# Optimization experiments

Measured on AMD Instinct MI355X. Metric: run time of the kernel, lower is better.

The kernel has to match this reference:

```python
import jax, jax.numpy as jnp
import numpy as np

EMBED_DIM = 1024
NUM_HEADS = 16
HEAD_DIM = EMBED_DIM // NUM_HEADS
SCALING = HEAD_DIM ** -0.5


def setup_inputs() -> dict:
    key = jax.random.key(0)
    ks = jax.random.split(key, 10)
    B, S, D = 2, 2048, EMBED_DIM
    lim = 1.0 / np.sqrt(D)  # torch Linear default init scale
    def lin(k):
        kw, kb = jax.random.split(k)
        W = jax.random.uniform(kw, (D, D), jnp.float32, -lim, lim)
        b = jax.random.uniform(kb, (D,), jnp.float32, -lim, lim)
        return W, b
    Wq, bq = lin(ks[0])
    Wk, bk = lin(ks[1])
    Wv, bv = lin(ks[2])
    Wo, bo = lin(ks[3])
    hidden_states = jax.random.normal(ks[4], (B, S, D), jnp.float32)
    attention_mask = jnp.ones((B, S), jnp.int32)  # unused by the module's forward
    return {"hidden_states": hidden_states, "attention_mask": attention_mask,
            "Wq": Wq, "bq": bq, "Wk": Wk, "bk": bk, "Wv": Wv, "bv": bv,
            "Wo": Wo, "bo": bo}


def reference(hidden_states, attention_mask, Wq, bq, Wk, bk, Wv, bv, Wo, bo):
    B, S, D = hidden_states.shape
    H, hd = NUM_HEADS, HEAD_DIM

    def split_heads(x):  # [B,S,D] -> [B,H,S,hd]
        return x.reshape(B, S, H, hd).transpose(0, 2, 1, 3)

    q = split_heads(hidden_states @ Wq.T + bq) * SCALING
    k = split_heads(hidden_states @ Wk.T + bk)
    v = split_heads(hidden_states @ Wv.T + bv)

    scores = jnp.einsum("bhqd,bhkd->bhqk", q, k)  # [B,H,S,S]
    mask_value = jnp.finfo(scores.dtype).min
    causal = jnp.triu(jnp.ones((S, S), bool), k=1)  # True above diagonal
    scores = jnp.where(causal, mask_value, scores)
    probs = jax.nn.softmax(scores, axis=-1)

    out = jnp.einsum("bhqk,bhkd->bhqd", probs, v)  # [B,H,S,hd]
    out = out.transpose(0, 2, 1, 3).reshape(B, S, D)
    return out @ Wo.T + bo
```

## Files before the change

kernel.cpp:

```cpp
#include <hip/hip_runtime.h>


typedef __bf16 bf16;
typedef __attribute__((ext_vector_type(8))) __bf16 bf16x8;
typedef __attribute__((ext_vector_type(4))) __bf16 bf16x4;
typedef __attribute__((ext_vector_type(4))) float f32x4;

#define MFMA16(a, b, c) __builtin_amdgcn_mfma_f32_16x16x32_bf16((a), (b), (c), 0, 0, 0)

__device__ __forceinline__ void gl_lds16(const bf16* g, bf16* l) {
  __builtin_amdgcn_global_load_lds(
      (__attribute__((address_space(1))) void*)g,
      (__attribute__((address_space(3))) void*)l, 16, 0, 0);
}

__global__ __launch_bounds__(256) void cvt5(
    const float* __restrict__ x, const float* __restrict__ wq,
    const float* __restrict__ wk, const float* __restrict__ wv,
    const float* __restrict__ wo,
    bf16* __restrict__ xb, bf16* __restrict__ wqb, bf16* __restrict__ wkb,
    bf16* __restrict__ wvb, bf16* __restrict__ wob) {
  const int bx = blockIdx.x;
  const float* s;
  bf16* d;
  int base;
  if (bx < 4096)      { s = x;  d = xb;  base = bx; }
  else if (bx < 5120) { s = wq; d = wqb; base = bx - 4096; }
  else if (bx < 6144) { s = wk; d = wkb; base = bx - 5120; }
  else if (bx < 7168) { s = wv; d = wvb; base = bx - 6144; }
  else                { s = wo; d = wob; base = bx - 7168; }
  const int i = base * 1024 + threadIdx.x * 4;
  const float4 v = *(const float4*)(s + i);
  bf16x4 o;
  o[0] = (bf16)v.x; o[1] = (bf16)v.y; o[2] = (bf16)v.z; o[3] = (bf16)v.w;
  *(bf16x4*)(d + i) = o;
}

__global__ __launch_bounds__(256) void vtrans(const bf16* __restrict__ v,
                                              bf16* __restrict__ vt) {
  __shared__ bf16 Ts[64 * 80];
  const int t = threadIdx.x;
  const int st = blockIdx.x;
  const int bh = blockIdx.y;
  const int bb = bh >> 4, h = bh & 15;
  const bf16* src = v + ((size_t)bb * 2048 + st * 64) * 1024 + h * 64;
#pragma unroll
  for (int i = 0; i < 2; ++i) {
    const int idx = i * 256 + t;
    const int sl = idx >> 3, c = idx & 7;
    *(bf16x8*)&Ts[sl * 80 + c * 8] = *(const bf16x8*)(src + (size_t)sl * 1024 + c * 8);
  }
  __syncthreads();
  bf16* dst = vt + (size_t)bh * 64 * 2048 + st * 64;
#pragma unroll
  for (int i = 0; i < 2; ++i) {
    const int idx = i * 256 + t;
    const int d = idx >> 3, c2 = idx & 7;
    bf16x8 tmp;
#pragma unroll
    for (int e = 0; e < 8; ++e) tmp[e] = Ts[(c2 * 8 + e) * 80 + d];
    *(bf16x8*)(dst + (size_t)d * 2048 + c2 * 8) = tmp;
  }
}

template <int BM, typename OutT>
__global__ __launch_bounds__(256, 2) void gemm_bt3(
    const bf16* __restrict__ A,
    const bf16* __restrict__ W0, const bf16* __restrict__ W1, const bf16* __restrict__ W2,
    const float* __restrict__ B0, const float* __restrict__ B1, const float* __restrict__ B2,
    OutT* __restrict__ O0, OutT* __restrict__ O1, OutT* __restrict__ O2,
    float s0, float s1, float s2, int K) {
  constexpr int WM = BM / 32;
  __shared__ bf16 As[BM * 64];
  __shared__ bf16 Bs[128 * 64];

  const int t = threadIdx.x;
  const int lane = t & 63;
  const int wv = t >> 6;
  const int wm = wv & 1, wn = wv >> 1;
  const int qd = lane >> 4, ln = lane & 15;

  const int which = blockIdx.x >> 3;
  const bf16* W = (which == 0) ? W0 : (which == 1) ? W1 : W2;
  const float* Bi = (which == 0) ? B0 : (which == 1) ? B1 : B2;
  OutT* O = (which == 0) ? O0 : (which == 1) ? O1 : O2;
  const float scale = (which == 0) ? s0 : (which == 1) ? s1 : s2;

  const int n0 = (blockIdx.x & 7) * 128;
  const int m0 = blockIdx.y * BM;

  f32x4 acc[WM][4] = {};

  for (int k0 = 0; k0 < K; k0 += 64) {
#pragma unroll
    for (int i = 0; i < BM / 32; ++i) {
      const int s = i * 256 + t;
      const int row = s >> 3;
      const int c = (s & 7) ^ (row & 7);
      gl_lds16(A + (size_t)(m0 + row) * K + k0 + c * 8, &As[s * 8]);
    }
#pragma unroll
    for (int i = 0; i < 4; ++i) {
      const int s = i * 256 + t;
      const int row = s >> 3;
      const int c = (s & 7) ^ (row & 7);
      gl_lds16(W + (size_t)(n0 + row) * K + k0 + c * 8, &Bs[s * 8]);
    }
    __syncthreads();

#pragma unroll
    for (int ks = 0; ks < 2; ++ks) {
      bf16x8 af[WM], bw[4];
#pragma unroll
      for (int i = 0; i < WM; ++i) {
        const int r = wm * (BM / 2) + i * 16 + ln;
        af[i] = *(const bf16x8*)&As[r * 64 + (((ks * 4 + qd) ^ (ln & 7)) << 3)];
      }
#pragma unroll
      for (int j = 0; j < 4; ++j) {
        const int r = wn * 64 + j * 16 + ln;
        bw[j] = *(const bf16x8*)&Bs[r * 64 + (((ks * 4 + qd) ^ (ln & 7)) << 3)];
      }
#pragma unroll
      for (int i = 0; i < WM; ++i)
#pragma unroll
        for (int j = 0; j < 4; ++j)
          acc[i][j] = MFMA16(af[i], bw[j], acc[i][j]);
    }
    __syncthreads();
  }

#pragma unroll
  for (int i = 0; i < WM; ++i) {
    const int row = m0 + wm * (BM / 2) + i * 16 + qd * 4;
#pragma unroll
    for (int j = 0; j < 4; ++j) {
      const int col = n0 + wn * 64 + j * 16 + ln;
      const float bias = Bi[col];
#pragma unroll
      for (int r = 0; r < 4; ++r) {
        const float v = (acc[i][j][r] + bias) * scale;
        O[(size_t)(row + r) * 1024 + col] = (OutT)v;
      }
    }
  }
}

__global__ __launch_bounds__(256, 4) void attn_causal(
    const bf16* __restrict__ Q, const bf16* __restrict__ Kg,
    const bf16* __restrict__ VT, bf16* __restrict__ Ob) {
  __shared__ bf16 Ks[2][64 * 64];
  __shared__ bf16 Vts[2][64 * 64];
  __shared__ bf16 Ps[4][16 * 64];

  const int t = threadIdx.x;
  const int lane = t & 63;
  const int w = t >> 6;
  const int qd = lane >> 4, ln = lane & 15;

  const int blk = blockIdx.x;
  const int bh = blk & 31;
  const int g = blk >> 5;
  const int a = g & 7, b = g >> 3;
  const int tq = (b == 0) ? (31 - a) : (b == 1) ? (16 + a) : (b == 2) ? (15 - a) : a;
  const int bb = bh >> 4, h = bh & 15;
  const size_t rowbase = (size_t)bb * 2048;
  const bf16* vtb = VT + (size_t)bh * 64 * 2048;

  const int q0 = tq * 64;
  const int nj = tq + 1;

  auto stage = [&](int buf, int j) {
    const bf16* kp = Kg + (rowbase + j * 64) * 1024 + h * 64;
#pragma unroll
    for (int i = 0; i < 2; ++i) {
      const int s = i * 256 + t;
      const int kv = s >> 3;
      const int c = (s & 7) ^ (kv & 7);
      gl_lds16(kp + (size_t)kv * 1024 + c * 8, &Ks[buf][s * 8]);
    }
#pragma unroll
    for (int i = 0; i < 2; ++i) {
      const int s = i * 256 + t;
      const int d = s >> 3;
      const int c = (s & 7) ^ (d & 7);
      gl_lds16(vtb + (size_t)d * 2048 + j * 64 + c * 8, &Vts[buf][s * 8]);
    }
  };

  const bf16* qp = Q + (rowbase + q0 + w * 16) * 1024 + h * 64;
  bf16x8 qf[2];
#pragma unroll
  for (int ks = 0; ks < 2; ++ks)
    qf[ks] = *(const bf16x8*)(qp + (size_t)ln * 1024 + ks * 32 + qd * 8);

  float l_run[4] = {0.f, 0.f, 0.f, 0.f};
  f32x4 accO[4] = {};

  stage(0, 0);

#pragma unroll 1
  for (int j = 0; j < nj; ++j) {
    const int buf = j & 1;
    __syncthreads();
    if (j + 1 < nj) stage(buf ^ 1, j + 1);

    f32x4 accS[4] = {};
#pragma unroll
    for (int ks = 0; ks < 2; ++ks) {
#pragma unroll
      for (int nt = 0; nt < 4; ++nt) {
        const bf16x8 bk = *(const bf16x8*)
            &Ks[buf][(nt * 16 + ln) * 64 + (((ks * 4 + qd) ^ (ln & 7)) << 3)];
        accS[nt] = MFMA16(qf[ks], bk, accS[nt]);
      }
    }

    if (j == nj - 1) {
#pragma unroll
      for (int r = 0; r < 4; ++r) {
        const int row = qd * 4 + r;
        const int qg = q0 + w * 16 + row;
        float sum = 0.f;
#pragma unroll
        for (int nt = 0; nt < 4; ++nt) {
          float p = __expf(accS[nt][r]);
          const int col = nt * 16 + ln;
          if ((j * 64 + col) > qg) p = 0.f;
          sum += p;
          Ps[w][row * 64 + ((((col >> 3) ^ (row & 7))) << 3) + (col & 7)] = (bf16)p;
        }
        l_run[r] += sum;
      }
    } else {
#pragma unroll
      for (int r = 0; r < 4; ++r) {
        const int row = qd * 4 + r;
        float sum = 0.f;
#pragma unroll
        for (int nt = 0; nt < 4; ++nt) {
          const float p = __expf(accS[nt][r]);
          const int col = nt * 16 + ln;
          sum += p;
          Ps[w][row * 64 + ((((col >> 3) ^ (row & 7))) << 3) + (col & 7)] = (bf16)p;
        }
        l_run[r] += sum;
      }
    }

#pragma unroll
    for (int kt = 0; kt < 2; ++kt) {
      const bf16x8 ap = *(const bf16x8*)
          &Ps[w][ln * 64 + (((kt * 4 + qd) ^ (ln & 7)) << 3)];
#pragma unroll
      for (int nt = 0; nt < 4; ++nt) {
        const bf16x8 bv = *(const bf16x8*)
            &Vts[buf][(nt * 16 + ln) * 64 + (((kt * 4 + qd) ^ (ln & 7)) << 3)];
        accO[nt] = MFMA16(ap, bv, accO[nt]);
      }
    }
  }

  bf16* op = Ob + (rowbase + q0 + w * 16) * 1024 + h * 64;
#pragma unroll
  for (int r = 0; r < 4; ++r) {
    float l = l_run[r];
#pragma unroll
    for (int off = 1; off < 16; off <<= 1) l += __shfl_xor(l, off, 64);
    const float inv_l = 1.0f / l;
#pragma unroll
    for (int nt = 0; nt < 4; ++nt)
      op[(size_t)(qd * 4 + r) * 1024 + nt * 16 + ln] = (bf16)(accO[nt][r] * inv_l);
  }
}

extern "C" void kernel_launch(void* const* d_in, const int* in_sizes, int n_in,
                              void* d_out, int out_size, void* d_ws, size_t ws_size,
                              hipStream_t stream) {
  const float* X  = (const float*)d_in[0];
  const float* Wq = (const float*)d_in[2];
  const float* bq = (const float*)d_in[3];
  const float* Wk = (const float*)d_in[4];
  const float* bk = (const float*)d_in[5];
  const float* Wv = (const float*)d_in[6];
  const float* bv = (const float*)d_in[7];
  const float* Wo = (const float*)d_in[8];
  const float* bo = (const float*)d_in[9];
  float* out = (float*)d_out;

  bf16* xb  = (bf16*)d_ws;
  bf16* wqb = xb  + (size_t)4096 * 1024;
  bf16* wkb = wqb + (size_t)1024 * 1024;
  bf16* wvb = wkb + (size_t)1024 * 1024;
  bf16* wob = wvb + (size_t)1024 * 1024;
  bf16* q   = wob + (size_t)1024 * 1024;
  bf16* k   = q   + (size_t)4096 * 1024;
  bf16* v   = k   + (size_t)4096 * 1024;
  bf16* vt  = v   + (size_t)4096 * 1024;
  bf16* ao  = xb;

  const float scaling = 0.125f;

  dim3 blk(256);
  cvt5<<<dim3(8192), blk, 0, stream>>>(X, Wq, Wk, Wv, Wo, xb, wqb, wkb, wvb, wob);
  gemm_bt3<128, bf16><<<dim3(24, 32), blk, 0, stream>>>(
      xb, wqb, wkb, wvb, bq, bk, bv, q, k, v, scaling, 1.f, 1.f, 1024);
  vtrans<<<dim3(32, 32), blk, 0, stream>>>(v, vt);
  attn_causal<<<dim3(1024), blk, 0, stream>>>(q, k, vt, ao);
  gemm_bt3<64, float><<<dim3(8, 64), blk, 0, stream>>>(
      ao, wob, wob, wob, bo, bo, bo, out, out, out, 1.f, 1.f, 1.f, 1024);
}
```

Measured before the change: 190.4 us.

## Fuse fp32-to-bf16 conversion into GEMM loads and use exp2 softmax

Removes the separate conversion kernel. The QKV and output-projection GEMMs now stream fp32 X and weights straight into LDS and convert to bf16 while building MFMA fragments. The K step halves to 32, and each GEMM now moves fp32 data, so global and LDS traffic per tile doubles, but a full launch and the conversion round trip to memory go away. The log2(e) factor is folded into the Q scaling so softmax can use exp2f instead of __expf.

```diff
diff --git a/kernel.cpp b/kernel.cpp
--- a/kernel.cpp
+++ b/kernel.cpp
@@ -3,37 +3,164 @@
 
 typedef __bf16 bf16;
 typedef __attribute__((ext_vector_type(8))) __bf16 bf16x8;
-typedef __attribute__((ext_vector_type(4))) __bf16 bf16x4;
 typedef __attribute__((ext_vector_type(4))) float f32x4;
 
 #define MFMA16(a, b, c) __builtin_amdgcn_mfma_f32_16x16x32_bf16((a), (b), (c), 0, 0, 0)
 
-__device__ __forceinline__ void gl_lds16(const bf16* g, bf16* l) {
+__device__ __forceinline__ void gl_lds16(const void* g, void* l) {
   __builtin_amdgcn_global_load_lds(
-      (__attribute__((address_space(1))) void*)g,
+      (const __attribute__((address_space(1))) void*)g,
       (__attribute__((address_space(3))) void*)l, 16, 0, 0);
 }
 
-__global__ __launch_bounds__(256) void cvt5(
-    const float* __restrict__ x, const float* __restrict__ wq,
-    const float* __restrict__ wk, const float* __restrict__ wv,
-    const float* __restrict__ wo,
-    bf16* __restrict__ xb, bf16* __restrict__ wqb, bf16* __restrict__ wkb,
-    bf16* __restrict__ wvb, bf16* __restrict__ wob) {
-  const int bx = blockIdx.x;
-  const float* s;
-  bf16* d;
-  int base;
-  if (bx < 4096)      { s = x;  d = xb;  base = bx; }
-  else if (bx < 5120) { s = wq; d = wqb; base = bx - 4096; }
-  else if (bx < 6144) { s = wk; d = wkb; base = bx - 5120; }
-  else if (bx < 7168) { s = wv; d = wvb; base = bx - 6144; }
-  else                { s = wo; d = wob; base = bx - 7168; }
-  const int i = base * 1024 + threadIdx.x * 4;
-  const float4 v = *(const float4*)(s + i);
-  bf16x4 o;
-  o[0] = (bf16)v.x; o[1] = (bf16)v.y; o[2] = (bf16)v.z; o[3] = (bf16)v.w;
-  *(bf16x4*)(d + i) = o;
+__device__ __forceinline__ bf16x8 rd_f32frag(const float* Ls, int row, int qd) {
+  const int x = row & 7;
+  const float4 a = *(const float4*)&Ls[row * 32 + ((((2 * qd)     ^ x)) << 2)];
+  const float4 b = *(const float4*)&Ls[row * 32 + ((((2 * qd + 1) ^ x)) << 2)];
+  bf16x8 r;
+  r[0] = (bf16)a.x; r[1] = (bf16)a.y; r[2] = (bf16)a.z; r[3] = (bf16)a.w;
+  r[4] = (bf16)b.x; r[5] = (bf16)b.y; r[6] = (bf16)b.z; r[7] = (bf16)b.w;
+  return r;
+}
+
+__global__ __launch_bounds__(256, 3) void gemm_qkv(
+    const float* __restrict__ X,
+    const float* __restrict__ W0, const float* __restrict__ W1, const float* __restrict__ W2,
+    const float* __restrict__ B0, const float* __restrict__ B1, const float* __restrict__ B2,
+    bf16* __restrict__ O0, bf16* __restrict__ O1, bf16* __restrict__ O2,
+    float s0) {
+  __shared__ float As[128 * 32];
+  __shared__ float Bs[128 * 32];
+
+  const int t = threadIdx.x;
+  const int lane = t & 63;
+  const int wv = t >> 6;
+  const int wm = wv & 1, wn = wv >> 1;
+  const int qd = lane >> 4, ln = lane & 15;
+
+  const int which = blockIdx.x >> 3;
+  const float* W = (which == 0) ? W0 : (which == 1) ? W1 : W2;
+  const float* Bi = (which == 0) ? B0 : (which == 1) ? B1 : B2;
+  bf16* O = (which == 0) ? O0 : (which == 1) ? O1 : O2;
+  const float scale = (which == 0) ? s0 : 1.0f;
+
+  const int n0 = (blockIdx.x & 7) * 128;
+  const int m0 = blockIdx.y * 128;
+  const int K = 1024;
+
+  f32x4 acc[4][4] = {};
+
+  for (int k0 = 0; k0 < K; k0 += 32) {
+#pragma unroll
+    for (int i = 0; i < 4; ++i) {
+      const int s = i * 256 + t;
+      const int row = s >> 3;
+      const int c = (s & 7) ^ (row & 7);
+      gl_lds16(X + (size_t)(m0 + row) * K + k0 + c * 4, &As[s * 4]);
+    }
+#pragma unroll
+    for (int i = 0; i < 4; ++i) {
+      const int s = i * 256 + t;
+      const int row = s >> 3;
+      const int c = (s & 7) ^ (row & 7);
+      gl_lds16(W + (size_t)(n0 + row) * K + k0 + c * 4, &Bs[s * 4]);
+    }
+    __syncthreads();
+
+    bf16x8 af[4], bw[4];
+#pragma unroll
+    for (int i = 0; i < 4; ++i)
+      af[i] = rd_f32frag(As, wm * 64 + i * 16 + ln, qd);
+#pragma unroll
+    for (int j = 0; j < 4; ++j)
+      bw[j] = rd_f32frag(Bs, wn * 64 + j * 16 + ln, qd);
+#pragma unroll
+    for (int i = 0; i < 4; ++i)
+#pragma unroll
+      for (int j = 0; j < 4; ++j)
+        acc[i][j] = MFMA16(af[i], bw[j], acc[i][j]);
+    __syncthreads();
+  }
+
+#pragma unroll
+  for (int i = 0; i < 4; ++i) {
+    const int row = m0 + wm * 64 + i * 16 + qd * 4;
+#pragma unroll
+    for (int j = 0; j < 4; ++j) {
+      const int col = n0 + wn * 64 + j * 16 + ln;
+      const float bias = Bi[col];
+#pragma unroll
+      for (int r = 0; r < 4; ++r) {
+        const float v = (acc[i][j][r] + bias) * scale;
+        O[(size_t)(row + r) * 1024 + col] = (bf16)v;
+      }
+    }
+  }
+}
+
+__global__ __launch_bounds__(256, 2) void gemm_o(
+    const bf16* __restrict__ A, const float* __restrict__ W,
+    const float* __restrict__ Bi, float* __restrict__ O) {
+  __shared__ bf16 As[64 * 32];
+  __shared__ float Bs[128 * 32];
+
+  const int t = threadIdx.x;
+  const int lane = t & 63;
+  const int wv = t >> 6;
+  const int wm = wv & 1, wn = wv >> 1;
+  const int qd = lane >> 4, ln = lane & 15;
+
+  const int n0 = blockIdx.x * 128;
+  const int m0 = blockIdx.y * 64;
+  const int K = 1024;
+
+  f32x4 acc[2][4] = {};
+
+  for (int k0 = 0; k0 < K; k0 += 32) {
+    {
+      const int s = t;
+      const int row = s >> 2;
+      const int c = (s & 3) ^ (row & 3);
+      gl_lds16(A + (size_t)(m0 + row) * K + k0 + c * 8, &As[s * 8]);
+    }
+#pragma unroll
+    for (int i = 0; i < 4; ++i) {
+      const int s = i * 256 + t;
+      const int row = s >> 3;
+      const int c = (s & 7) ^ (row & 7);
+      gl_lds16(W + (size_t)(n0 + row) * K + k0 + c * 4, &Bs[s * 4]);
+    }
+    __syncthreads();
+
+    bf16x8 af[2], bw[4];
+#pragma unroll
+    for (int i = 0; i < 2; ++i) {
+      const int row = wm * 32 + i * 16 + ln;
+      af[i] = *(const bf16x8*)&As[row * 32 + ((qd ^ (row & 3)) << 3)];
+    }
+#pragma unroll
+    for (int j = 0; j < 4; ++j)
+      bw[j] = rd_f32frag(Bs, wn * 64 + j * 16 + ln, qd);
+#pragma unroll
+    for (int i = 0; i < 2; ++i)
+#pragma unroll
+      for (int j = 0; j < 4; ++j)
+        acc[i][j] = MFMA16(af[i], bw[j], acc[i][j]);
+    __syncthreads();
+  }
+
+#pragma unroll
+  for (int i = 0; i < 2; ++i) {
+    const int row = m0 + wm * 32 + i * 16 + qd * 4;
+#pragma unroll
+    for (int j = 0; j < 4; ++j) {
+      const int col = n0 + wn * 64 + j * 16 + ln;
+      const float bias = Bi[col];
+#pragma unroll
+      for (int r = 0; r < 4; ++r)
+        O[(size_t)(row + r) * 1024 + col] = acc[i][j][r] + bias;
+    }
+  }
 }
 
 __global__ __launch_bounds__(256) void vtrans(const bf16* __restrict__ v,
@@ -63,89 +190,6 @@
   }
 }
 
-template <int BM, typename OutT>
-__global__ __launch_bounds__(256, 2) void gemm_bt3(
-    const bf16* __restrict__ A,
-    const bf16* __restrict__ W0, const bf16* __restrict__ W1, const bf16* __restrict__ W2,
-    const float* __restrict__ B0, const float* __restrict__ B1, const float* __restrict__ B2,
-    OutT* __restrict__ O0, OutT* __restrict__ O1, OutT* __restrict__ O2,
-    float s0, float s1, float s2, int K) {
-  constexpr int WM = BM / 32;
-  __shared__ bf16 As[BM * 64];
-  __shared__ bf16 Bs[128 * 64];
-
-  const int t = threadIdx.x;
-  const int lane = t & 63;
-  const int wv = t >> 6;
-  const int wm = wv & 1, wn = wv >> 1;
-  const int qd = lane >> 4, ln = lane & 15;
-
-  const int which = blockIdx.x >> 3;
-  const bf16* W = (which == 0) ? W0 : (which == 1) ? W1 : W2;
-  const float* Bi = (which == 0) ? B0 : (which == 1) ? B1 : B2;
-  OutT* O = (which == 0) ? O0 : (which == 1) ? O1 : O2;
-  const float scale = (which == 0) ? s0 : (which == 1) ? s1 : s2;
-
-  const int n0 = (blockIdx.x & 7) * 128;
-  const int m0 = blockIdx.y * BM;
-
-  f32x4 acc[WM][4] = {};
-
-  for (int k0 = 0; k0 < K; k0 += 64) {
-#pragma unroll
-    for (int i = 0; i < BM / 32; ++i) {
-      const int s = i * 256 + t;
-      const int row = s >> 3;
-      const int c = (s & 7) ^ (row & 7);
-      gl_lds16(A + (size_t)(m0 + row) * K + k0 + c * 8, &As[s * 8]);
-    }
-#pragma unroll
-    for (int i = 0; i < 4; ++i) {
-      const int s = i * 256 + t;
-      const int row = s >> 3;
-      const int c = (s & 7) ^ (row & 7);
-      gl_lds16(W + (size_t)(n0 + row) * K + k0 + c * 8, &Bs[s * 8]);
-    }
-    __syncthreads();
-
-#pragma unroll
-    for (int ks = 0; ks < 2; ++ks) {
-      bf16x8 af[WM], bw[4];
-#pragma unroll
-      for (int i = 0; i < WM; ++i) {
-        const int r = wm * (BM / 2) + i * 16 + ln;
-        af[i] = *(const bf16x8*)&As[r * 64 + (((ks * 4 + qd) ^ (ln & 7)) << 3)];
-      }
-#pragma unroll
-      for (int j = 0; j < 4; ++j) {
-        const int r = wn * 64 + j * 16 + ln;
-        bw[j] = *(const bf16x8*)&Bs[r * 64 + (((ks * 4 + qd) ^ (ln & 7)) << 3)];
-      }
-#pragma unroll
-      for (int i = 0; i < WM; ++i)
-#pragma unroll
-        for (int j = 0; j < 4; ++j)
-          acc[i][j] = MFMA16(af[i], bw[j], acc[i][j]);
-    }
-    __syncthreads();
-  }
-
-#pragma unroll
-  for (int i = 0; i < WM; ++i) {
-    const int row = m0 + wm * (BM / 2) + i * 16 + qd * 4;
-#pragma unroll
-    for (int j = 0; j < 4; ++j) {
-      const int col = n0 + wn * 64 + j * 16 + ln;
-      const float bias = Bi[col];
-#pragma unroll
-      for (int r = 0; r < 4; ++r) {
-        const float v = (acc[i][j][r] + bias) * scale;
-        O[(size_t)(row + r) * 1024 + col] = (OutT)v;
-      }
-    }
-  }
-}
-
 __global__ __launch_bounds__(256, 4) void attn_causal(
     const bf16* __restrict__ Q, const bf16* __restrict__ Kg,
     const bf16* __restrict__ VT, bf16* __restrict__ Ob) {
@@ -224,7 +268,7 @@
         float sum = 0.f;
 #pragma unroll
         for (int nt = 0; nt < 4; ++nt) {
-          float p = __expf(accS[nt][r]);
+          float p = exp2f(accS[nt][r]);
           const int col = nt * 16 + ln;
           if ((j * 64 + col) > qg) p = 0.f;
           sum += p;
@@ -239,7 +283,7 @@
         float sum = 0.f;
 #pragma unroll
         for (int nt = 0; nt < 4; ++nt) {
-          const float p = __expf(accS[nt][r]);
+          const float p = exp2f(accS[nt][r]);
           const int col = nt * 16 + ln;
           sum += p;
           Ps[w][row * 64 + ((((col >> 3) ^ (row & 7))) << 3) + (col & 7)] = (bf16)p;
@@ -288,25 +332,18 @@
   const float* bo = (const float*)d_in[9];
   float* out = (float*)d_out;
 
-  bf16* xb  = (bf16*)d_ws;
-  bf16* wqb = xb  + (size_t)4096 * 1024;
-  bf16* wkb = wqb + (size_t)1024 * 1024;
-  bf16* wvb = wkb + (size_t)1024 * 1024;
-  bf16* wob = wvb + (size_t)1024 * 1024;
-  bf16* q   = wob + (size_t)1024 * 1024;
-  bf16* k   = q   + (size_t)4096 * 1024;
-  bf16* v   = k   + (size_t)4096 * 1024;
-  bf16* vt  = v   + (size_t)4096 * 1024;
-  bf16* ao  = xb;
-
-  const float scaling = 0.125f;
+  bf16* q  = (bf16*)d_ws;
+  bf16* k  = q  + (size_t)4096 * 1024;
+  bf16* v  = k  + (size_t)4096 * 1024;
+  bf16* vt = v  + (size_t)4096 * 1024;
+  bf16* ao = vt + (size_t)4096 * 1024;
+
+  const float qscale = 0.125f * 1.4426950408889634f;
 
   dim3 blk(256);
-  cvt5<<<dim3(8192), blk, 0, stream>>>(X, Wq, Wk, Wv, Wo, xb, wqb, wkb, wvb, wob);
-  gemm_bt3<128, bf16><<<dim3(24, 32), blk, 0, stream>>>(
-      xb, wqb, wkb, wvb, bq, bk, bv, q, k, v, scaling, 1.f, 1.f, 1024);
+  gemm_qkv<<<dim3(24, 32), blk, 0, stream>>>(
+      X, Wq, Wk, Wv, bq, bk, bv, q, k, v, qscale);
   vtrans<<<dim3(32, 32), blk, 0, stream>>>(v, vt);
   attn_causal<<<dim3(1024), blk, 0, stream>>>(q, k, vt, ao);
-  gemm_bt3<64, float><<<dim3(8, 64), blk, 0, stream>>>(
-      ao, wob, wob, wob, bo, bo, bo, out, out, out, 1.f, 1.f, 1.f, 1024);
-}
+  gemm_o<<<dim3(8, 64), blk, 0, stream>>>(ao, Wo, bo, out);
+}
```

New measurement: 212.8 us. 11.8% more time.

## Use 2 waves per attention block with 32 query rows each and exp2

Applied to the files above, without the earlier changes.

The causal attention kernel now runs with 128 threads (2 waves), and each wave handles 32 query rows as two 16-row M-tiles. Each K and V fragment loaded from LDS is reused across two MFMAs, which halves LDS reads per FLOP. The log2(e) factor is folded into the Q projection scale so the softmax can use exp2f. The change raises register pressure per wave and lowers the wave count per block, which may cut latency hiding, and launch bounds are relaxed to 2 blocks per CU.

```diff
diff --git a/kernel.cpp b/kernel.cpp
--- a/kernel.cpp
+++ b/kernel.cpp
@@ -146,12 +146,12 @@
   }
 }
 
-__global__ __launch_bounds__(256, 4) void attn_causal(
+__global__ __launch_bounds__(128, 2) void attn_causal(
     const bf16* __restrict__ Q, const bf16* __restrict__ Kg,
     const bf16* __restrict__ VT, bf16* __restrict__ Ob) {
   __shared__ bf16 Ks[2][64 * 64];
   __shared__ bf16 Vts[2][64 * 64];
-  __shared__ bf16 Ps[4][16 * 64];
+  __shared__ bf16 Ps[2][32 * 64];
 
   const int t = threadIdx.x;
   const int lane = t & 63;
@@ -173,29 +173,31 @@
   auto stage = [&](int buf, int j) {
     const bf16* kp = Kg + (rowbase + j * 64) * 1024 + h * 64;
 #pragma unroll
-    for (int i = 0; i < 2; ++i) {
-      const int s = i * 256 + t;
+    for (int i = 0; i < 4; ++i) {
+      const int s = i * 128 + t;
       const int kv = s >> 3;
       const int c = (s & 7) ^ (kv & 7);
       gl_lds16(kp + (size_t)kv * 1024 + c * 8, &Ks[buf][s * 8]);
     }
 #pragma unroll
-    for (int i = 0; i < 2; ++i) {
-      const int s = i * 256 + t;
+    for (int i = 0; i < 4; ++i) {
+      const int s = i * 128 + t;
       const int d = s >> 3;
       const int c = (s & 7) ^ (d & 7);
       gl_lds16(vtb + (size_t)d * 2048 + j * 64 + c * 8, &Vts[buf][s * 8]);
     }
   };
 
-  const bf16* qp = Q + (rowbase + q0 + w * 16) * 1024 + h * 64;
-  bf16x8 qf[2];
+  const bf16* qp = Q + (rowbase + q0 + w * 32) * 1024 + h * 64;
+  bf16x8 qf[2][2];
 #pragma unroll
   for (int ks = 0; ks < 2; ++ks)
-    qf[ks] = *(const bf16x8*)(qp + (size_t)ln * 1024 + ks * 32 + qd * 8);
-
-  float l_run[4] = {0.f, 0.f, 0.f, 0.f};
-  f32x4 accO[4] = {};
+#pragma unroll
+    for (int mt = 0; mt < 2; ++mt)
+      qf[ks][mt] = *(const bf16x8*)(qp + (size_t)(mt * 16 + ln) * 1024 + ks * 32 + qd * 8);
+
+  float l_run[2][4] = {};
+  f32x4 accO[2][4] = {};
 
   stage(0, 0);
 
@@ -205,73 +207,87 @@
     __syncthreads();
     if (j + 1 < nj) stage(buf ^ 1, j + 1);
 
-    f32x4 accS[4] = {};
+    f32x4 accS[2][4] = {};
 #pragma unroll
     for (int ks = 0; ks < 2; ++ks) {
 #pragma unroll
       for (int nt = 0; nt < 4; ++nt) {
         const bf16x8 bk = *(const bf16x8*)
             &Ks[buf][(nt * 16 + ln) * 64 + (((ks * 4 + qd) ^ (ln & 7)) << 3)];
-        accS[nt] = MFMA16(qf[ks], bk, accS[nt]);
+        accS[0][nt] = MFMA16(qf[ks][0], bk, accS[0][nt]);
+        accS[1][nt] = MFMA16(qf[ks][1], bk, accS[1][nt]);
       }
     }
 
     if (j == nj - 1) {
 #pragma unroll
-      for (int r = 0; r < 4; ++r) {
-        const int row = qd * 4 + r;
-        const int qg = q0 + w * 16 + row;
-        float sum = 0.f;
-#pragma unroll
-        for (int nt = 0; nt < 4; ++nt) {
-          float p = __expf(accS[nt][r]);
-          const int col = nt * 16 + ln;
-          if ((j * 64 + col) > qg) p = 0.f;
-          sum += p;
-          Ps[w][row * 64 + ((((col >> 3) ^ (row & 7))) << 3) + (col & 7)] = (bf16)p;
+      for (int mt = 0; mt < 2; ++mt)
+#pragma unroll
+        for (int r = 0; r < 4; ++r) {
+          const int row = mt * 16 + qd * 4 + r;
+          const int qg = q0 + w * 32 + row;
+          float sum = 0.f;
+#pragma unroll
+          for (int nt = 0; nt < 4; ++nt) {
+            float p = exp2f(accS[mt][nt][r]);
+            const int col = nt * 16 + ln;
+            if ((j * 64 + col) > qg) p = 0.f;
+            sum += p;
+            Ps[w][row * 64 + ((((col >> 3) ^ (row & 7))) << 3) + (col & 7)] = (bf16)p;
+          }
+          l_run[mt][r] += sum;
         }
-        l_run[r] += sum;
-      }
     } else {
 #pragma unroll
-      for (int r = 0; r < 4; ++r) {
-        const int row = qd * 4 + r;
-        float sum = 0.f;
-#pragma unroll
-        for (int nt = 0; nt < 4; ++nt) {
-          const float p = __expf(accS[nt][r]);
-          const int col = nt * 16 + ln;
-          sum += p;
-          Ps[w][row * 64 + ((((col >> 3) ^ (row & 7))) << 3) + (col & 7)] = (bf16)p;
+      for (int mt = 0; mt < 2; ++mt)
+#pragma unroll
+        for (int r = 0; r < 4; ++r) {
+          const int row = mt * 16 + qd * 4 + r;
+          float sum = 0.f;
+#pragma unroll
+          for (int nt = 0; nt < 4; ++nt) {
+            const float p = exp2f(accS[mt][nt][r]);
+            const int col = nt * 16 + ln;
+            sum += p;
+            Ps[w][row * 64 + ((((col >> 3) ^ (row & 7))) << 3) + (col & 7)] = (bf16)p;
+          }
+          l_run[mt][r] += sum;
         }
-        l_run[r] += sum;
-      }
     }
 
 #pragma unroll
     for (int kt = 0; kt < 2; ++kt) {
-      const bf16x8 ap = *(const bf16x8*)
-          &Ps[w][ln * 64 + (((kt * 4 + qd) ^ (ln & 7)) << 3)];
+      bf16x8 ap[2];
+#pragma unroll
+      for (int mt = 0; mt < 2; ++mt) {
+        const int row = mt * 16 + ln;
+        ap[mt] = *(const bf16x8*)
+            &Ps[w][row * 64 + (((kt * 4 + qd) ^ (row & 7)) << 3)];
+      }
 #pragma unroll
       for (int nt = 0; nt < 4; ++nt) {
         const bf16x8 bv = *(const bf16x8*)
             &Vts[buf][(nt * 16 + ln) * 64 + (((kt * 4 + qd) ^ (ln & 7)) << 3)];
-        accO[nt] = MFMA16(ap, bv, accO[nt]);
-      }
-    }
-  }
-
-  bf16* op = Ob + (rowbase + q0 + w * 16) * 1024 + h * 64;
-#pragma unroll
-  for (int r = 0; r < 4; ++r) {
-    float l = l_run[r];
-#pragma unroll
-    for (int off = 1; off < 16; off <<= 1) l += __shfl_xor(l, off, 64);
-    const float inv_l = 1.0f / l;
-#pragma unroll
-    for (int nt = 0; nt < 4; ++nt)
-      op[(size_t)(qd * 4 + r) * 1024 + nt * 16 + ln] = (bf16)(accO[nt][r] * inv_l);
-  }
+        accO[0][nt] = MFMA16(ap[0], bv, accO[0][nt]);
+        accO[1][nt] = MFMA16(ap[1], bv, accO[1][nt]);
+      }
+    }
+  }
+
+  bf16* op = Ob + (rowbase + q0 + w * 32) * 1024 + h * 64;
+#pragma unroll
+  for (int mt = 0; mt < 2; ++mt)
+#pragma unroll
+    for (int r = 0; r < 4; ++r) {
+      float l = l_run[mt][r];
+#pragma unroll
+      for (int off = 1; off < 16; off <<= 1) l += __shfl_xor(l, off, 64);
+      const float inv_l = 1.0f / l;
+#pragma unroll
+      for (int nt = 0; nt < 4; ++nt)
+        op[(size_t)(mt * 16 + qd * 4 + r) * 1024 + nt * 16 + ln] =
+            (bf16)(accO[mt][nt][r] * inv_l);
+    }
 }
 
 extern "C" void kernel_launch(void* const* d_in, const int* in_sizes, int n_in,
@@ -299,14 +315,14 @@
   bf16* vt  = v   + (size_t)4096 * 1024;
   bf16* ao  = xb;
 
-  const float scaling = 0.125f;
+  const float qscale = 0.125f * 1.4426950408889634f;
 
   dim3 blk(256);
   cvt5<<<dim3(8192), blk, 0, stream>>>(X, Wq, Wk, Wv, Wo, xb, wqb, wkb, wvb, wob);
   gemm_bt3<128, bf16><<<dim3(24, 32), blk, 0, stream>>>(
-      xb, wqb, wkb, wvb, bq, bk, bv, q, k, v, scaling, 1.f, 1.f, 1024);
+      xb, wqb, wkb, wvb, bq, bk, bv, q, k, v, qscale, 1.f, 1.f, 1024);
   vtrans<<<dim3(32, 32), blk, 0, stream>>>(v, vt);
-  attn_causal<<<dim3(1024), blk, 0, stream>>>(q, k, vt, ao);
+  attn_causal<<<dim3(1024), dim3(128), 0, stream>>>(q, k, vt, ao);
   gemm_bt3<64, float><<<dim3(8, 64), blk, 0, stream>>>(
       ao, wob, wob, wob, bo, bo, bo, out, out, out, 1.f, 1.f, 1.f, 1024);
 }
```

New measurement: 201.8 us. 1.06x slower.
